# Kernel optimization log

Hardware: AMD Instinct MI355X
Metric: run time of the kernel (lower is better)

The kernel has to match this reference:

```python
import jax, jax.numpy as jnp
import numpy as np

# Static graph-batch geometry: B graphs, N nodes each (contiguous), DEG avg degree.
B, N, DEG = 128, 512, 16
GID, GH = 128, 128      # g_in_dim, g_hidden_dim
CID, CE = 64, 64        # c_in_dim, c_embed_dim
HAZ = 256               # haz_dim
K1, K2, K3 = 256, 128, 64


def _gcn(x, src, dst, mask, W, b, n):
    # GCN layer with self loops over masked (surviving) nodes; masked-out nodes contribute nothing.
    h = x @ W  # [n, GH]
    w = mask[src] * mask[dst]                                  # edge alive iff both endpoints alive
    deg = mask + jax.ops.segment_sum(w, dst, num_segments=n)    # +mask = self loop
    dinv = jax.lax.rsqrt(jnp.maximum(deg, 1.0))
    norm = w * dinv[src] * dinv[dst]
    agg = jax.ops.segment_sum(norm[:, None] * h[src], dst, num_segments=n)
    self_term = h * (mask * dinv * dinv)[:, None]               # self-loop norm = 1/deg
    return (agg + self_term + b) * mask[:, None]


def _pool(x, mask, p, k):
    # Score-based top-k pooling (MVPool score -> gate -> keep top ratio per graph), mask-based for static shapes.
    score = jax.nn.sigmoid((x @ p) / jnp.sqrt(jnp.sum(p * p)))  # [B*N]
    s = jnp.where(mask > 0, score, -jnp.inf).reshape(B, N)
    _, idx = jax.lax.top_k(s, k)                                 # [B, k]
    new_mask = jnp.zeros((B, N), x.dtype).at[jnp.arange(B)[:, None], idx].set(1.0).reshape(-1)
    x = x * (score * new_mask)[:, None]
    return x, new_mask


def _readout(x, mask):
    # readout='both': concat(global_max_pool, global_mean_pool) per graph.
    xm = x.reshape(B, N, -1)
    m = mask.reshape(B, N, 1)
    mx = jnp.max(jnp.where(m > 0, xm, -1e30), axis=1)
    avg = jnp.sum(xm * m, axis=1) / jnp.maximum(jnp.sum(m, axis=1), 1.0)
    return jnp.concatenate([mx, avg], axis=1)


def _forward(x, inp_c, src, dst, W1, b1, W2, b2, W3, b3, p1, p2, p3, We, Wa, ba, Wb, bb, Wc):
    n = B * N
    mask = jnp.ones((n,), x.dtype)
    x = jax.nn.relu(_gcn(x, src, dst, mask, W1, b1, n))
    x, mask = _pool(x, mask, p1, K1)
    x1 = _readout(x, mask)
    x = jax.nn.relu(_gcn(x, src, dst, mask, W2, b2, n))
    x, mask = _pool(x, mask, p2, K2)
    x2 = _readout(x, mask)
    x = jax.nn.relu(_gcn(x, src, dst, mask, W3, b3, n))
    x, mask = _pool(x, mask, p3, K3)
    x3 = _readout(x, mask)
    hg = jax.nn.relu(x1) + jax.nn.relu(x2) + jax.nn.relu(x3)     # [B, 2*GH]
    embed = jax.nn.relu(inp_c @ We)                               # [B, CE]
    fusion = jnp.concatenate([embed, hg], axis=1)                 # [B, 320]
    h = jax.nn.relu(fusion @ Wa + ba)                             # dropout skipped (eval mode)
    h = jax.nn.relu(h @ Wb + bb)
    return h @ Wc                                                 # out_dim=1 -> Identity


def setup_inputs() -> dict:
    key = jax.random.key(0)
    ks = jax.random.split(key, 16)
    n = B * N
    x = jax.random.normal(ks[0], (n, GID), jnp.float32)
    inp_c = jax.random.normal(ks[1], (B, CID), jnp.float32)
    offs = (jnp.arange(B, dtype=jnp.int32) * N)[:, None]
    src = (jax.random.randint(ks[2], (B, N * DEG), 0, N, jnp.int32) + offs).reshape(-1)
    dst = (jax.random.randint(ks[3], (B, N * DEG), 0, N, jnp.int32) + offs).reshape(-1)
    edge_index = jnp.stack([src, dst])
    batch = jnp.arange(n, dtype=jnp.int32) // N
    def lin(k, i, o):
        return jax.random.normal(k, (i, o), jnp.float32) / np.float32(np.sqrt(i))
    return dict(
        x=x, inp_c=inp_c, edge_index=edge_index, batch=batch,
        W1=lin(ks[4], GID, GH), b1=jnp.zeros((GH,), jnp.float32),
        W2=lin(ks[5], GH, GH), b2=jnp.zeros((GH,), jnp.float32),
        W3=lin(ks[6], GH, GH), b3=jnp.zeros((GH,), jnp.float32),
        p1=jax.random.normal(ks[7], (GH,), jnp.float32),
        p2=jax.random.normal(ks[8], (GH,), jnp.float32),
        p3=jax.random.normal(ks[9], (GH,), jnp.float32),
        We=lin(ks[10], CID, CE),
        Wa=lin(ks[11], 2 * GH + CE, HAZ), ba=jnp.zeros((HAZ,), jnp.float32),
        Wb=lin(ks[12], HAZ, HAZ // 2), bb=jnp.zeros((HAZ // 2,), jnp.float32),
        Wc=lin(ks[13], HAZ // 2, 1),
    )


def reference(x, inp_c, edge_index, batch, W1, b1, W2, b2, W3, b3, p1, p2, p3, We, Wa, ba, Wb, bb, Wc):
    # batch is implicitly arange(n)//N (contiguous equal-size graphs); reductions use the reshape form.
    src, dst = edge_index[0], edge_index[1]
    return _forward(x, inp_c, src, dst, W1, b1, W2, b2, W3, b3, p1, p2, p3, We, Wa, ba, Wb, bb, Wc)
```

## Files before the change

kernel.cpp:

```cpp
#include <hip/hip_runtime.h>
#include <math.h>

#define NNODE 65536
#define NEDGE 1048576
#define NGRAPH 128
#define NPG 512
#define EPG 8192

typedef _Float16 f16x8 __attribute__((ext_vector_type(8)));
typedef _Float16 f16x4 __attribute__((ext_vector_type(4)));
typedef float f32x4 __attribute__((ext_vector_type(4)));


__global__ __launch_bounds__(512) void k_csr(const int* __restrict__ srcE, const int* __restrict__ dstE,
                                             int* __restrict__ rp, int* __restrict__ csr,
                                             float* __restrict__ gate, int* __restrict__ alive,
                                             float* __restrict__ dinv, float* __restrict__ hg,
                                             const float* __restrict__ W0, const float* __restrict__ W1,
                                             const float* __restrict__ W2, _Float16* __restrict__ wh,
                                             _Float16* __restrict__ wl,
                                             const float* __restrict__ p0, const float* __restrict__ p1,
                                             const float* __restrict__ p2, float* __restrict__ qinv) {
    __shared__ int cnt[512];
    __shared__ int wsum[8];
    int t = threadIdx.x;
    if (blockIdx.x >= 128) {
        int vb = (blockIdx.x - 128) * 2 + (t >> 8);
        int tt = t & 255;
        if (vb == 192) {
            if (tt < 192) {
                int w = tt >> 6, lane = tt & 63;
                const float* P = (w == 0) ? p0 : (w == 1) ? p1 : p2;
                float s = P[lane] * P[lane] + P[lane + 64] * P[lane + 64];
                for (int m = 32; m >= 1; m >>= 1) s += __shfl_xor(s, m);
                if (lane == 0) qinv[w] = rsqrtf(s);
            }
        } else if (vb < 192) {
            int l = vb >> 6;
            int e = (vb & 63) * 256 + tt;
            const float* W = (l == 0) ? W0 : (l == 1) ? W1 : W2;
            int k = e >> 7, n = e & 127;
            float w = W[e];
            _Float16 hi = (_Float16)w;
            _Float16 lo = (_Float16)((w - (float)hi) * 2048.0f);
            int nt = n >> 4, nn = n & 15, ks = k >> 5, quad = (k & 31) >> 3, j = k & 7;
            int off = l * 16384 + ((nt * 4 + ks) * 64 + (quad * 16 + nn)) * 8 + j;
            wh[off] = hi;
            wl[off] = lo;
        }
        return;
    }
    int g = blockIdx.x;
    int nd = g * NPG + t;
    cnt[t] = 0;
    gate[nd] = 1.f;
    alive[nd] = nd;
    if (t < 256) hg[g * 256 + t] = 0.f;
    __syncthreads();
    int ebase = g * EPG;
    int dl[16];
    for (int i = 0; i < 16; ++i) {
        int e = ebase + t + i * 512;
        int d = dstE[e] - g * NPG;
        dl[i] = d;
        atomicAdd(&cnt[d], 1);
    }
    __syncthreads();
    int v = cnt[t];
    dinv[nd] = rsqrtf(1.f + (float)v);
    int lane = t & 63, wid = t >> 6;
    int x = v;
    for (int o = 1; o < 64; o <<= 1) {
        int n = __shfl_up(x, o);
        if (lane >= o) x += n;
    }
    if (lane == 63) wsum[wid] = x;
    __syncthreads();
    if (t == 0) {
        int run = 0;
        for (int i = 0; i < 8; ++i) { int s = wsum[i]; wsum[i] = run; run += s; }
    }
    __syncthreads();
    int incl = x + wsum[wid];
    int excl = incl - v;
    rp[nd] = ebase + excl;
    if (g == NGRAPH - 1 && t == 511) rp[NNODE] = NEDGE;
    cnt[t] = excl;
    __syncthreads();
    for (int i = 0; i < 16; ++i) {
        int e = ebase + t + i * 512;
        int pos = atomicAdd(&cnt[dl[i]], 1);
        csr[ebase + pos] = srcE[e];
    }
}


#define CVT8(hi8, lo8, a0, a1, a2, a3, a4, a5, a6, a7)                         \
    {                                                                           \
        _Float16 q0 = (_Float16)a0, q1 = (_Float16)a1, q2 = (_Float16)a2,       \
                 q3 = (_Float16)a3, q4 = (_Float16)a4, q5 = (_Float16)a5,       \
                 q6 = (_Float16)a6, q7 = (_Float16)a7;                          \
        hi8 = (f16x8){q0, q1, q2, q3, q4, q5, q6, q7};                          \
        lo8 = (f16x8){(_Float16)((a0 - (float)q0) * 2048.f),                    \
                      (_Float16)((a1 - (float)q1) * 2048.f),                    \
                      (_Float16)((a2 - (float)q2) * 2048.f),                    \
                      (_Float16)((a3 - (float)q3) * 2048.f),                    \
                      (_Float16)((a4 - (float)q4) * 2048.f),                    \
                      (_Float16)((a5 - (float)q5) * 2048.f),                    \
                      (_Float16)((a6 - (float)q6) * 2048.f),                    \
                      (_Float16)((a7 - (float)q7) * 2048.f)};                   \
    }

__global__ __launch_bounds__(256, 2) void k_gemm(const float* __restrict__ x0, const _Float16* __restrict__ xh,
                                                 const _Float16* __restrict__ xl, const _Float16* __restrict__ wh,
                                                 const _Float16* __restrict__ wl, const float* __restrict__ gate,
                                                 const int* __restrict__ alive, float* __restrict__ h,
                                                 int srcF32, int perg) {
    __shared__ _Float16 aH[128 * 72];
    __shared__ _Float16 aL[128 * 72];
    __shared__ _Float16 bH[8192];
    __shared__ _Float16 bL[8192];
    int t = threadIdx.x;
    int lane = t & 63;
    int wv = t >> 6;
    int quad = lane >> 4, mm = lane & 15;
    int gg = blockIdx.x & 127;
    int cc0 = blockIdx.x >> 7;
    int rowbase = gg * perg + cc0 * 128;

    f32x4 accH[2][8], accM[2][8];
    for (int a = 0; a < 2; ++a)
        for (int b = 0; b < 8; ++b) {
            accH[a][b] = (f32x4){0.f, 0.f, 0.f, 0.f};
            accM[a][b] = (f32x4){0.f, 0.f, 0.f, 0.f};
        }

    for (int kh = 0; kh < 2; ++kh) {
        if (kh) __syncthreads();
        for (int pp = 0; pp < 4; ++pp) {
            int seg = t + pp * 256;
            int nt = seg >> 7, ksl = (seg >> 6) & 1, ln = seg & 63;
            int goff = ((nt * 4 + kh * 2 + ksl) * 64 + ln) * 8;
            *(uint4*)(bH + seg * 8) = *(const uint4*)(wh + goff);
            *(uint4*)(bL + seg * 8) = *(const uint4*)(wl + goff);
        }
        for (int pp = 0; pp < 4; ++pp) {
            int c = t + pp * 256;
            int r = c >> 3, ch = c & 7;
            int node = alive[rowbase + r];
            size_t src = (size_t)node * 128 + kh * 64 + ch * 8;
            f16x8 hi8, lo8;
            if (srcF32) {
                float4 v0 = *(const float4*)(x0 + src);
                float4 v1 = *(const float4*)(x0 + src + 4);
                CVT8(hi8, lo8, v0.x, v0.y, v0.z, v0.w, v1.x, v1.y, v1.z, v1.w);
            } else {
                hi8 = *(const f16x8*)(xh + src);
                lo8 = *(const f16x8*)(xl + src);
            }
            *(f16x8*)(aH + r * 72 + ch * 8) = hi8;
            *(f16x8*)(aL + r * 72 + ch * 8) = lo8;
        }
        __syncthreads();

        for (int ksl = 0; ksl < 2; ++ksl) {
            f16x8 Ah[2], Al[2];
            for (int mt = 0; mt < 2; ++mt) {
                int row = wv * 32 + mt * 16 + mm;
                Ah[mt] = *(const f16x8*)(aH + row * 72 + ksl * 32 + quad * 8);
                Al[mt] = *(const f16x8*)(aL + row * 72 + ksl * 32 + quad * 8);
            }
            for (int nt = 0; nt < 8; ++nt) {
                f16x8 Bh = *(const f16x8*)(bH + ((nt * 2 + ksl) * 64 + lane) * 8);
                f16x8 Bl = *(const f16x8*)(bL + ((nt * 2 + ksl) * 64 + lane) * 8);
                for (int mt = 0; mt < 2; ++mt) {
                    accH[mt][nt] = __builtin_amdgcn_mfma_f32_16x16x32_f16(Ah[mt], Bh, accH[mt][nt], 0, 0, 0);
                    accM[mt][nt] = __builtin_amdgcn_mfma_f32_16x16x32_f16(Ah[mt], Bl, accM[mt][nt], 0, 0, 0);
                    accM[mt][nt] = __builtin_amdgcn_mfma_f32_16x16x32_f16(Al[mt], Bh, accM[mt][nt], 0, 0, 0);
                }
            }
        }
    }

    for (int mt = 0; mt < 2; ++mt)
        for (int i = 0; i < 4; ++i) {
            int rl = wv * 32 + mt * 16 + quad * 4 + i;
            int node = alive[rowbase + rl];
            float g = gate[node];
            float* hr = h + (size_t)node * 128 + mm;
            for (int nt = 0; nt < 8; ++nt)
                hr[nt * 16] = g * (accH[mt][nt][i] + accM[mt][nt][i] * (1.f / 2048.f));
        }
}


__global__ __launch_bounds__(1024) void k_aggL(const float* __restrict__ h, const float* __restrict__ dinv,
                                               const int* __restrict__ rp, const int* __restrict__ csr,
                                               const int* __restrict__ alive, const float* __restrict__ bias,
                                               const float* __restrict__ p, _Float16* __restrict__ xh,
                                               _Float16* __restrict__ xl, float* __restrict__ spart, int Kp) {
    __shared__ float hsl[512 * 68];
    __shared__ float dinv_l[512];
    __shared__ float2 nbw[64][16];
    __shared__ float bias_l[64];
    __shared__ float p_l[64];
    int t = threadIdx.x;
    int g = blockIdx.x & 127;
    int fh = blockIdx.x >> 7;
    int fb = fh * 64;
    int gbase = g * NPG;

    for (int r0 = 0; r0 < 512; r0 += 128) {
        int r = r0 + (t >> 3);
        int f8 = (t & 7) * 8;
        const float* src = h + (size_t)(gbase + r) * 128 + fb + f8;
        float4 v0 = *(const float4*)(src);
        float4 v1 = *(const float4*)(src + 4);
        *(float4*)(hsl + r * 68 + f8) = v0;
        *(float4*)(hsl + r * 68 + f8 + 4) = v1;
    }
    if (t < 512) dinv_l[t] = dinv[gbase + t];
    if (t < 64) { bias_l[t] = bias[fb + t]; p_l[t] = p[fb + t]; }
    __syncthreads();

    int lane16 = t & 15;
    int qid = t >> 4;

    for (int idx = qid; idx < Kp; idx += 64) {
        int d = alive[g * Kp + idx];
        int rd = d - gbase;
        int jb = rp[d], je = rp[d + 1];
        float dvd = dinv_l[rd];
        float4 hd = *(const float4*)(hsl + rd * 68 + lane16 * 4);
        float4 acc;
        acc.x = dvd * hd.x; acc.y = dvd * hd.y; acc.z = dvd * hd.z; acc.w = dvd * hd.w;

        for (int bk = jb; bk < je; bk += 16) {
            int nk = je - bk; if (nk > 16) nk = 16;
            float wv = 0.f;
            int rs = rd;
            if (lane16 < nk) {
                rs = csr[bk + lane16] - gbase;
                wv = dinv_l[rs];
            }
            nbw[qid][lane16] = make_float2(wv, __int_as_float(rs));
            int nk4 = (nk + 3) & ~3;
            for (int k = 0; k < nk4; k += 4) {
                float2 e0 = nbw[qid][k];
                float2 e1 = nbw[qid][k + 1];
                float2 e2 = nbw[qid][k + 2];
                float2 e3 = nbw[qid][k + 3];
                float4 h0 = *(const float4*)(hsl + __float_as_int(e0.y) * 68 + lane16 * 4);
                float4 h1 = *(const float4*)(hsl + __float_as_int(e1.y) * 68 + lane16 * 4);
                float4 h2 = *(const float4*)(hsl + __float_as_int(e2.y) * 68 + lane16 * 4);
                float4 h3 = *(const float4*)(hsl + __float_as_int(e3.y) * 68 + lane16 * 4);
                acc.x = fmaf(e0.x, h0.x, acc.x); acc.y = fmaf(e0.x, h0.y, acc.y);
                acc.z = fmaf(e0.x, h0.z, acc.z); acc.w = fmaf(e0.x, h0.w, acc.w);
                acc.x = fmaf(e1.x, h1.x, acc.x); acc.y = fmaf(e1.x, h1.y, acc.y);
                acc.z = fmaf(e1.x, h1.z, acc.z); acc.w = fmaf(e1.x, h1.w, acc.w);
                acc.x = fmaf(e2.x, h2.x, acc.x); acc.y = fmaf(e2.x, h2.y, acc.y);
                acc.z = fmaf(e2.x, h2.z, acc.z); acc.w = fmaf(e2.x, h2.w, acc.w);
                acc.x = fmaf(e3.x, h3.x, acc.x); acc.y = fmaf(e3.x, h3.y, acc.y);
                acc.z = fmaf(e3.x, h3.z, acc.z); acc.w = fmaf(e3.x, h3.w, acc.w);
            }
        }

        float4 b4 = *(const float4*)(bias_l + lane16 * 4);
        float4 o;
        o.x = fmaxf(fmaf(dvd, acc.x, b4.x), 0.f);
        o.y = fmaxf(fmaf(dvd, acc.y, b4.y), 0.f);
        o.z = fmaxf(fmaf(dvd, acc.z, b4.z), 0.f);
        o.w = fmaxf(fmaf(dvd, acc.w, b4.w), 0.f);

        _Float16 q0 = (_Float16)o.x, q1 = (_Float16)o.y, q2 = (_Float16)o.z, q3 = (_Float16)o.w;
        f16x4 oh = {q0, q1, q2, q3};
        f16x4 ol = {(_Float16)((o.x - (float)q0) * 2048.f), (_Float16)((o.y - (float)q1) * 2048.f),
                    (_Float16)((o.z - (float)q2) * 2048.f), (_Float16)((o.w - (float)q3) * 2048.f)};
        *(f16x4*)(xh + (size_t)d * 128 + fb + lane16 * 4) = oh;
        *(f16x4*)(xl + (size_t)d * 128 + fb + lane16 * 4) = ol;

        float4 p4 = *(const float4*)(p_l + lane16 * 4);
        float ps = o.x * p4.x + o.y * p4.y + o.z * p4.z + o.w * p4.w;
        ps += __shfl_xor(ps, 1);
        ps += __shfl_xor(ps, 2);
        ps += __shfl_xor(ps, 4);
        ps += __shfl_xor(ps, 8);
        if (lane16 == 0) spart[(size_t)fh * NNODE + d] = ps;
    }
}


__global__ __launch_bounds__(1024) void k_aggS(const float* __restrict__ h, const float* __restrict__ dinv,
                                               const int* __restrict__ rp, const int* __restrict__ csr,
                                               const int* __restrict__ alive, const float* __restrict__ bias,
                                               const float* __restrict__ p, _Float16* __restrict__ xh,
                                               _Float16* __restrict__ xl, float* __restrict__ spart, int Kp) {
    __shared__ float slab[256 * 68];
    __shared__ float dinv_l[512];
    __shared__ int   map_l[512];
    __shared__ float2 nbw[64][16];
    __shared__ float bias_l[64];
    __shared__ float p_l[64];
    int t = threadIdx.x;
    int g = blockIdx.x & 127;
    int fh = blockIdx.x >> 7;
    int fb = fh * 64;
    int gbase = g * NPG;

    if (t < 512) { dinv_l[t] = dinv[gbase + t]; map_l[t] = 0; }
    if (t < 64) { bias_l[t] = bias[fb + t]; p_l[t] = p[fb + t]; }
    for (int r0 = 0; r0 < Kp; r0 += 128) {
        int r = r0 + (t >> 3);
        if (r < Kp) {
            int node = alive[g * Kp + r];
            int f8 = (t & 7) * 8;
            const float* src = h + (size_t)node * 128 + fb + f8;
            float4 v0 = *(const float4*)(src);
            float4 v1 = *(const float4*)(src + 4);
            *(float4*)(slab + r * 68 + f8) = v0;
            *(float4*)(slab + r * 68 + f8 + 4) = v1;
        }
    }
    __syncthreads();
    if (t < Kp) map_l[alive[g * Kp + t] - gbase] = t;
    __syncthreads();

    int lane16 = t & 15;
    int qid = t >> 4;

    for (int idx = qid; idx < Kp; idx += 64) {
        int d = alive[g * Kp + idx];
        int rd = d - gbase;
        int jb = rp[d], je = rp[d + 1];
        float dvd = dinv_l[rd];
        float4 hd = *(const float4*)(slab + idx * 68 + lane16 * 4);
        float4 acc;
        acc.x = dvd * hd.x; acc.y = dvd * hd.y; acc.z = dvd * hd.z; acc.w = dvd * hd.w;

        for (int bk = jb; bk < je; bk += 16) {
            int nk = je - bk; if (nk > 16) nk = 16;
            float wv = 0.f;
            int sl = idx;
            if (lane16 < nk) {
                int rs = csr[bk + lane16] - gbase;
                wv = dinv_l[rs];
                sl = map_l[rs];
            }
            nbw[qid][lane16] = make_float2(wv, __int_as_float(sl));
            int nk4 = (nk + 3) & ~3;
            for (int k = 0; k < nk4; k += 4) {
                float2 e0 = nbw[qid][k];
                float2 e1 = nbw[qid][k + 1];
                float2 e2 = nbw[qid][k + 2];
                float2 e3 = nbw[qid][k + 3];
                float4 h0 = *(const float4*)(slab + __float_as_int(e0.y) * 68 + lane16 * 4);
                float4 h1 = *(const float4*)(slab + __float_as_int(e1.y) * 68 + lane16 * 4);
                float4 h2 = *(const float4*)(slab + __float_as_int(e2.y) * 68 + lane16 * 4);
                float4 h3 = *(const float4*)(slab + __float_as_int(e3.y) * 68 + lane16 * 4);
                acc.x = fmaf(e0.x, h0.x, acc.x); acc.y = fmaf(e0.x, h0.y, acc.y);
                acc.z = fmaf(e0.x, h0.z, acc.z); acc.w = fmaf(e0.x, h0.w, acc.w);
                acc.x = fmaf(e1.x, h1.x, acc.x); acc.y = fmaf(e1.x, h1.y, acc.y);
                acc.z = fmaf(e1.x, h1.z, acc.z); acc.w = fmaf(e1.x, h1.w, acc.w);
                acc.x = fmaf(e2.x, h2.x, acc.x); acc.y = fmaf(e2.x, h2.y, acc.y);
                acc.z = fmaf(e2.x, h2.z, acc.z); acc.w = fmaf(e2.x, h2.w, acc.w);
                acc.x = fmaf(e3.x, h3.x, acc.x); acc.y = fmaf(e3.x, h3.y, acc.y);
                acc.z = fmaf(e3.x, h3.z, acc.z); acc.w = fmaf(e3.x, h3.w, acc.w);
            }
        }

        float4 b4 = *(const float4*)(bias_l + lane16 * 4);
        float4 o;
        o.x = fmaxf(fmaf(dvd, acc.x, b4.x), 0.f);
        o.y = fmaxf(fmaf(dvd, acc.y, b4.y), 0.f);
        o.z = fmaxf(fmaf(dvd, acc.z, b4.z), 0.f);
        o.w = fmaxf(fmaf(dvd, acc.w, b4.w), 0.f);

        _Float16 q0 = (_Float16)o.x, q1 = (_Float16)o.y, q2 = (_Float16)o.z, q3 = (_Float16)o.w;
        f16x4 oh = {q0, q1, q2, q3};
        f16x4 ol = {(_Float16)((o.x - (float)q0) * 2048.f), (_Float16)((o.y - (float)q1) * 2048.f),
                    (_Float16)((o.z - (float)q2) * 2048.f), (_Float16)((o.w - (float)q3) * 2048.f)};
        *(f16x4*)(xh + (size_t)d * 128 + fb + lane16 * 4) = oh;
        *(f16x4*)(xl + (size_t)d * 128 + fb + lane16 * 4) = ol;

        float4 p4 = *(const float4*)(p_l + lane16 * 4);
        float ps = o.x * p4.x + o.y * p4.y + o.z * p4.z + o.w * p4.w;
        ps += __shfl_xor(ps, 1);
        ps += __shfl_xor(ps, 2);
        ps += __shfl_xor(ps, 4);
        ps += __shfl_xor(ps, 8);
        if (lane16 == 0) spart[(size_t)fh * NNODE + d] = ps;
    }
}


__device__ __forceinline__ void pool_body(const _Float16* __restrict__ xh, const _Float16* __restrict__ xl,
                                          const float* __restrict__ spart, const float* __restrict__ qinv,
                                          int lidx, float* __restrict__ gate,
                                          int* __restrict__ alive, float* __restrict__ hg,
                                          const int* __restrict__ rp, const int* __restrict__ csr,
                                          float* __restrict__ dinv, int K, int last, int g, int t) {
    __shared__ unsigned hist[1024];
    __shared__ unsigned wsum[8];
    __shared__ float cand[512];
    __shared__ int ad[256];
    __shared__ float ag[256];
    __shared__ float red[1024];
    __shared__ int m_new[512];
    __shared__ int scnt;
    __shared__ unsigned ccnt;
    __shared__ unsigned tbb, tbab;
    __shared__ float thrS;
    int gbase = g * NPG;
    int d = gbase + t;

    float odv = dinv[d];
    int m = odv > 0.f;
    float z = spart[d] + spart[NNODE + d];
    float sc = 1.f / (1.f + expf(-z * qinv[lidx]));
    unsigned bits = m ? __float_as_uint(sc) : 0u;
    unsigned bucket = bits >> 21;
    hist[t] = 0; hist[t + 512] = 0;
    if (t == 0) { scnt = 0; ccnt = 0; }
    __syncthreads();
    atomicAdd(&hist[bucket], 1u);
    __syncthreads();
    unsigned a0 = hist[1023 - 2 * t];
    unsigned a1 = hist[1022 - 2 * t];
    unsigned pair = a0 + a1;
    unsigned v = pair;
    for (int o = 1; o < 64; o <<= 1) {
        unsigned n = __shfl_up(v, o);
        if ((t & 63) >= o) v += n;
    }
    if ((t & 63) == 63) wsum[t >> 6] = v;
    __syncthreads();
    if (t == 0) {
        unsigned run = 0;
        for (int i = 0; i < 8; ++i) { unsigned x = wsum[i]; wsum[i] = run; run += x; }
    }
    __syncthreads();
    unsigned incl = v + wsum[t >> 6];
    unsigned excl = incl - pair;
    unsigned uK = (unsigned)K;
    if (excl < uK && excl + a0 >= uK) { tbb = 1023 - 2 * t; tbab = excl; }
    else if (excl + a0 < uK && incl >= uK) { tbb = 1022 - 2 * t; tbab = excl + a0; }
    __syncthreads();
    unsigned bsel = tbb;
    unsigned r = uK - tbab;
    if (m && bucket == bsel) {
        unsigned pos = atomicAdd(&ccnt, 1u);
        cand[pos] = sc;
    }
    __syncthreads();
    unsigned c = ccnt;
    if (t < (int)c) {
        float vv = cand[t];
        unsigned gt = 0;
        for (unsigned i = 0; i < c; ++i) gt += (cand[i] > vv) ? 1u : 0u;
        if (gt == r - 1) thrS = vv;
    }
    __syncthreads();
    float thr = thrS;

    int nm = (m && sc >= thr) ? 1 : 0;
    gate[d] = nm ? sc : 0.f;
    m_new[t] = nm;
    if (nm) {
        int pos = atomicAdd(&scnt, 1);
        if (pos < K) {
            alive[g * K + pos] = d;
            ad[pos] = d;
            ag[pos] = sc;
        }
    }
    __syncthreads();

    if (!last) {
        float nd = 0.f;
        if (nm) {
            int jb = rp[d], je = rp[d + 1];
            int sum = 0;
            for (int j = jb; j < je; ++j) sum += m_new[csr[j] - gbase];
            nd = rsqrtf(1.f + (float)sum);
        }
        dinv[d] = nd;
    }

    int f = t & 127, c2 = t >> 7;
    float mx = 0.f, sm = 0.f;
#define REC(node) ((float)xh[(size_t)(node)*128 + f] + (float)xl[(size_t)(node)*128 + f] * (1.f / 2048.f))
    for (int j = c2; j < K; j += 16) {
        float v0 = REC(ad[j]) * ag[j];
        float v1 = REC(ad[j + 4]) * ag[j + 4];
        float v2 = REC(ad[j + 8]) * ag[j + 8];
        float v3 = REC(ad[j + 12]) * ag[j + 12];
        mx = fmaxf(fmaxf(fmaxf(mx, v0), fmaxf(v1, v2)), v3);
        sm += v0 + v1 + v2 + v3;
    }
#undef REC
    red[t] = mx; red[512 + t] = sm;
    __syncthreads();
    if (c2 == 0) {
        for (int cc = 1; cc < 4; ++cc) {
            mx = fmaxf(mx, red[cc * 128 + f]);
            sm += red[512 + cc * 128 + f];
        }
        hg[g * 256 + f] += mx;
        hg[g * 256 + 128 + f] += sm / (float)K;
    }
}


__global__ __launch_bounds__(512) void k_poolA(const _Float16* __restrict__ xh, const _Float16* __restrict__ xl,
                                               const float* __restrict__ spart, const float* __restrict__ qinv,
                                               int lidx, float* __restrict__ gate,
                                               int* __restrict__ alive, float* __restrict__ hg,
                                               const int* __restrict__ rp, const int* __restrict__ csr,
                                               float* __restrict__ dinv, int K, int last) {
    pool_body(xh, xl, spart, qinv, lidx, gate, alive, hg, rp, csr, dinv, K, last,
              blockIdx.x, threadIdx.x);
}


__global__ __launch_bounds__(512) void k_poolB(const _Float16* __restrict__ xh, const _Float16* __restrict__ xl,
                                               const float* __restrict__ spart, const float* __restrict__ qinv,
                                               int lidx, float* __restrict__ gate,
                                               int* __restrict__ alive, float* __restrict__ hg,
                                               const int* __restrict__ rp, const int* __restrict__ csr,
                                               float* __restrict__ dinv, int K, int last,
                                               const _Float16* __restrict__ wh3, const _Float16* __restrict__ wl3,
                                               float* __restrict__ h) {
    __shared__ _Float16 aH[128 * 72];
    __shared__ _Float16 aL[128 * 72];
    __shared__ _Float16 bH[8192];
    __shared__ _Float16 bL[8192];
    int t = threadIdx.x, g = blockIdx.x;
    pool_body(xh, xl, spart, qinv, lidx, gate, alive, hg, rp, csr, dinv, K, last, g, t);
    __syncthreads();

    int lane = t & 63;
    int wv = t >> 6;
    int quad = lane >> 4, mm = lane & 15;
    int rowbase = g * 128;

    f32x4 accH[2][8], accM[2][8];
    for (int a = 0; a < 2; ++a)
        for (int b = 0; b < 8; ++b) {
            accH[a][b] = (f32x4){0.f, 0.f, 0.f, 0.f};
            accM[a][b] = (f32x4){0.f, 0.f, 0.f, 0.f};
        }

    for (int kh = 0; kh < 2; ++kh) {
        if (kh) __syncthreads();
        for (int pp = 0; pp < 2; ++pp) {
            int seg = t + pp * 512;
            int nt = seg >> 7, ksl = (seg >> 6) & 1, ln = seg & 63;
            int goff = ((nt * 4 + kh * 2 + ksl) * 64 + ln) * 8;
            *(uint4*)(bH + seg * 8) = *(const uint4*)(wh3 + goff);
            *(uint4*)(bL + seg * 8) = *(const uint4*)(wl3 + goff);
        }
        for (int pp = 0; pp < 2; ++pp) {
            int c = t + pp * 512;
            int r = c >> 3, ch = c & 7;
            int node = alive[rowbase + r];
            size_t src = (size_t)node * 128 + kh * 64 + ch * 8;
            *(f16x8*)(aH + r * 72 + ch * 8) = *(const f16x8*)(xh + src);
            *(f16x8*)(aL + r * 72 + ch * 8) = *(const f16x8*)(xl + src);
        }
        __syncthreads();

        if (t < 256) {
            for (int ksl = 0; ksl < 2; ++ksl) {
                f16x8 Ah[2], Al[2];
                for (int mt = 0; mt < 2; ++mt) {
                    int row = wv * 32 + mt * 16 + mm;
                    Ah[mt] = *(const f16x8*)(aH + row * 72 + ksl * 32 + quad * 8);
                    Al[mt] = *(const f16x8*)(aL + row * 72 + ksl * 32 + quad * 8);
                }
                for (int nt = 0; nt < 8; ++nt) {
                    f16x8 Bh = *(const f16x8*)(bH + ((nt * 2 + ksl) * 64 + lane) * 8);
                    f16x8 Bl = *(const f16x8*)(bL + ((nt * 2 + ksl) * 64 + lane) * 8);
                    for (int mt = 0; mt < 2; ++mt) {
                        accH[mt][nt] = __builtin_amdgcn_mfma_f32_16x16x32_f16(Ah[mt], Bh, accH[mt][nt], 0, 0, 0);
                        accM[mt][nt] = __builtin_amdgcn_mfma_f32_16x16x32_f16(Ah[mt], Bl, accM[mt][nt], 0, 0, 0);
                        accM[mt][nt] = __builtin_amdgcn_mfma_f32_16x16x32_f16(Al[mt], Bh, accM[mt][nt], 0, 0, 0);
                    }
                }
            }
        }
    }

    if (t < 256) {
        for (int mt = 0; mt < 2; ++mt)
            for (int i = 0; i < 4; ++i) {
                int rl = wv * 32 + mt * 16 + quad * 4 + i;
                int node = alive[rowbase + rl];
                float gg = gate[node];
                float* hr = h + (size_t)node * 128 + mm;
                for (int nt = 0; nt < 8; ++nt)
                    hr[nt * 16] = gg * (accH[mt][nt][i] + accM[mt][nt][i] * (1.f / 2048.f));
            }
    }
}


__global__ __launch_bounds__(512) void k_poolC(const _Float16* __restrict__ xh, const _Float16* __restrict__ xl,
                                               const float* __restrict__ spart, const float* __restrict__ qinv,
                                               int lidx, float* __restrict__ gate,
                                               int* __restrict__ alive, float* __restrict__ hg,
                                               const int* __restrict__ rp, const int* __restrict__ csr,
                                               float* __restrict__ dinv, int K, int last,
                                               const float* __restrict__ inp_c,
                                               const float* __restrict__ We, const float* __restrict__ Wa,
                                               const float* __restrict__ ba, const float* __restrict__ Wb,
                                               const float* __restrict__ bb, const float* __restrict__ Wc,
                                               float* __restrict__ out) {
    __shared__ float fus[320];
    __shared__ float h1[256];
    __shared__ float h2[128];
    int t = threadIdx.x, g = blockIdx.x;
    pool_body(xh, xl, spart, qinv, lidx, gate, alive, hg, rp, csr, dinv, K, last, g, t);
    __syncthreads();

    if (t < 64) {
        float a = 0.f;
        for (int j = 0; j < 64; ++j) a = fmaf(inp_c[g * 64 + j], We[j * 64 + t], a);
        fus[t] = fmaxf(a, 0.f);
    }
    if (t < 256) fus[64 + t] = hg[g * 256 + t];
    __syncthreads();
    if (t < 256) {
        float a = ba[t];
        for (int j = 0; j < 320; ++j) a = fmaf(fus[j], Wa[j * 256 + t], a);
        h1[t] = fmaxf(a, 0.f);
    }
    __syncthreads();
    if (t < 128) {
        float a = bb[t];
        for (int j = 0; j < 256; ++j) a = fmaf(h1[j], Wb[j * 128 + t], a);
        h2[t] = fmaxf(a, 0.f);
    }
    __syncthreads();
    if (t == 0) {
        float a = 0.f;
        for (int j = 0; j < 128; ++j) a = fmaf(h2[j], Wc[j], a);
        out[g] = a;
    }
}


extern "C" void kernel_launch(void* const* d_in, const int* in_sizes, int n_in,
                              void* d_out, int out_size, void* d_ws, size_t ws_size,
                              hipStream_t stream) {
    (void)in_sizes; (void)n_in; (void)out_size; (void)ws_size;
    const float* x_in  = (const float*)d_in[0];
    const float* inp_c = (const float*)d_in[1];
    const int*   ei    = (const int*)d_in[2];
    const int* srcE = ei;
    const int* dstE = ei + NEDGE;
    const float* Wl[3] = {(const float*)d_in[4], (const float*)d_in[6], (const float*)d_in[8]};
    const float* bl[3] = {(const float*)d_in[5], (const float*)d_in[7], (const float*)d_in[9]};
    const float* Pl[3] = {(const float*)d_in[10], (const float*)d_in[11], (const float*)d_in[12]};
    const float* We = (const float*)d_in[13];
    const float* Wa = (const float*)d_in[14];
    const float* ba = (const float*)d_in[15];
    const float* Wb = (const float*)d_in[16];
    const float* bb = (const float*)d_in[17];
    const float* Wc = (const float*)d_in[18];
    float* out = (float*)d_out;

    char* w = (char*)d_ws;
    size_t off = 0;
    auto alloc = [&](size_t bytes) -> void* {
        void* p = w + off;
        off = (off + bytes + 255) & ~(size_t)255;
        return p;
    };
    int*   rp    = (int*)alloc((NNODE + 1) * 4);
    int*   csr   = (int*)alloc(NEDGE * 4);
    float* dinv  = (float*)alloc(NNODE * 4);
    float* gate  = (float*)alloc(NNODE * 4);
    float* spart = (float*)alloc((size_t)2 * NNODE * 4);
    float* qinv  = (float*)alloc(256);
    int*   alive = (int*)alloc(NNODE * 4);
    float* hbuf  = (float*)alloc((size_t)NNODE * 128 * 4);
    _Float16* xh = (_Float16*)alloc((size_t)NNODE * 128 * 2);
    _Float16* xl = (_Float16*)alloc((size_t)NNODE * 128 * 2);
    float* hg    = (float*)alloc(NGRAPH * 256 * 4);
    _Float16* wfh = (_Float16*)alloc(3 * 16384 * 2);
    _Float16* wfl = (_Float16*)alloc(3 * 16384 * 2);

    k_csr<<<225, 512, 0, stream>>>(srcE, dstE, rp, csr, gate, alive, dinv, hg,
                                   Wl[0], Wl[1], Wl[2], wfh, wfl, Pl[0], Pl[1], Pl[2], qinv);

    k_gemm<<<512, 256, 0, stream>>>(x_in, xh, xl, wfh, wfl, gate, alive, hbuf, 1, 512);
    k_aggL<<<256, 1024, 0, stream>>>(hbuf, dinv, rp, csr, alive, bl[0], Pl[0], xh, xl, spart, 512);
    k_poolA<<<NGRAPH, 512, 0, stream>>>(xh, xl, spart, qinv, 0, gate, alive, hg, rp, csr, dinv, 256, 0);

    k_gemm<<<256, 256, 0, stream>>>(x_in, xh, xl, wfh + 16384, wfl + 16384, gate, alive, hbuf, 0, 256);
    k_aggS<<<256, 1024, 0, stream>>>(hbuf, dinv, rp, csr, alive, bl[1], Pl[1], xh, xl, spart, 256);
    k_poolB<<<NGRAPH, 512, 0, stream>>>(xh, xl, spart, qinv, 1, gate, alive, hg, rp, csr, dinv, 128, 0,
                                        wfh + 32768, wfl + 32768, hbuf);

    k_aggS<<<256, 1024, 0, stream>>>(hbuf, dinv, rp, csr, alive, bl[2], Pl[2], xh, xl, spart, 128);
    k_poolC<<<NGRAPH, 512, 0, stream>>>(xh, xl, spart, qinv, 2, gate, alive, hg, rp, csr, dinv, 64, 1,
                                        inp_c, We, Wa, ba, Wb, bb, Wc, out);
}
```

Before: 263.0 us.

## Fuse layer-2 feature GEMM into first pooling kernel

The first pooling kernel now also computes the layer-2 GEMM for its graph's 256 surviving nodes. It gathers their split-f16 features and the weight fragments into shared memory, runs MFMA with hi/lo error compensation, and writes the gated result to hbuf. This removes a separate k_gemm launch and the global round-trip between pooling and the GEMM. The cost is that only 128 blocks with large LDS footprints (~106KB) do the GEMM, instead of 256 blocks, which may reduce parallelism.

```diff
diff --git a/kernel.cpp b/kernel.cpp
--- a/kernel.cpp
+++ b/kernel.cpp
@@ -516,9 +516,76 @@
                                                int lidx, float* __restrict__ gate,
                                                int* __restrict__ alive, float* __restrict__ hg,
                                                const int* __restrict__ rp, const int* __restrict__ csr,
-                                               float* __restrict__ dinv, int K, int last) {
-    pool_body(xh, xl, spart, qinv, lidx, gate, alive, hg, rp, csr, dinv, K, last,
-              blockIdx.x, threadIdx.x);
+                                               float* __restrict__ dinv, int K, int last,
+                                               const _Float16* __restrict__ wh2, const _Float16* __restrict__ wl2,
+                                               float* __restrict__ h) {
+    __shared__ _Float16 aH[256 * 72];
+    __shared__ _Float16 aL[256 * 72];
+    __shared__ _Float16 bH[8192];
+    __shared__ _Float16 bL[8192];
+    int t = threadIdx.x, g = blockIdx.x;
+    pool_body(xh, xl, spart, qinv, lidx, gate, alive, hg, rp, csr, dinv, K, last, g, t);
+    __syncthreads();
+
+    int lane = t & 63;
+    int wv = t >> 6;
+    int quad = lane >> 4, mm = lane & 15;
+    int rowbase = g * 256;
+
+    f32x4 accH[2][8], accM[2][8];
+    for (int a = 0; a < 2; ++a)
+        for (int b = 0; b < 8; ++b) {
+            accH[a][b] = (f32x4){0.f, 0.f, 0.f, 0.f};
+            accM[a][b] = (f32x4){0.f, 0.f, 0.f, 0.f};
+        }
+
+    for (int kh = 0; kh < 2; ++kh) {
+        if (kh) __syncthreads();
+        for (int pp = 0; pp < 2; ++pp) {
+            int seg = t + pp * 512;
+            int nt = seg >> 7, ksl = (seg >> 6) & 1, ln = seg & 63;
+            int goff = ((nt * 4 + kh * 2 + ksl) * 64 + ln) * 8;
+            *(uint4*)(bH + seg * 8) = *(const uint4*)(wh2 + goff);
+            *(uint4*)(bL + seg * 8) = *(const uint4*)(wl2 + goff);
+        }
+        for (int pp = 0; pp < 4; ++pp) {
+            int c = t + pp * 512;
+            int r = c >> 3, ch = c & 7;
+            int node = alive[rowbase + r];
+            size_t src = (size_t)node * 128 + kh * 64 + ch * 8;
+            *(f16x8*)(aH + r * 72 + ch * 8) = *(const f16x8*)(xh + src);
+            *(f16x8*)(aL + r * 72 + ch * 8) = *(const f16x8*)(xl + src);
+        }
+        __syncthreads();
+
+        for (int ksl = 0; ksl < 2; ++ksl) {
+            f16x8 Ah[2], Al[2];
+            for (int mt = 0; mt < 2; ++mt) {
+                int row = wv * 32 + mt * 16 + mm;
+                Ah[mt] = *(const f16x8*)(aH + row * 72 + ksl * 32 + quad * 8);
+                Al[mt] = *(const f16x8*)(aL + row * 72 + ksl * 32 + quad * 8);
+            }
+            for (int nt = 0; nt < 8; ++nt) {
+                f16x8 Bh = *(const f16x8*)(bH + ((nt * 2 + ksl) * 64 + lane) * 8);
+                f16x8 Bl = *(const f16x8*)(bL + ((nt * 2 + ksl) * 64 + lane) * 8);
+                for (int mt = 0; mt < 2; ++mt) {
+                    accH[mt][nt] = __builtin_amdgcn_mfma_f32_16x16x32_f16(Ah[mt], Bh, accH[mt][nt], 0, 0, 0);
+                    accM[mt][nt] = __builtin_amdgcn_mfma_f32_16x16x32_f16(Ah[mt], Bl, accM[mt][nt], 0, 0, 0);
+                    accM[mt][nt] = __builtin_amdgcn_mfma_f32_16x16x32_f16(Al[mt], Bh, accM[mt][nt], 0, 0, 0);
+                }
+            }
+        }
+    }
+
+    for (int mt = 0; mt < 2; ++mt)
+        for (int i = 0; i < 4; ++i) {
+            int rl = wv * 32 + mt * 16 + quad * 4 + i;
+            int node = alive[rowbase + rl];
+            float gg = gate[node];
+            float* hr = h + (size_t)node * 128 + mm;
+            for (int nt = 0; nt < 8; ++nt)
+                hr[nt * 16] = gg * (accH[mt][nt][i] + accM[mt][nt][i] * (1.f / 2048.f));
+        }
 }
 
 
@@ -695,9 +762,9 @@
 
     k_gemm<<<512, 256, 0, stream>>>(x_in, xh, xl, wfh, wfl, gate, alive, hbuf, 1, 512);
     k_aggL<<<256, 1024, 0, stream>>>(hbuf, dinv, rp, csr, alive, bl[0], Pl[0], xh, xl, spart, 512);
-    k_poolA<<<NGRAPH, 512, 0, stream>>>(xh, xl, spart, qinv, 0, gate, alive, hg, rp, csr, dinv, 256, 0);
-
-    k_gemm<<<256, 256, 0, stream>>>(x_in, xh, xl, wfh + 16384, wfl + 16384, gate, alive, hbuf, 0, 256);
+    k_poolA<<<NGRAPH, 512, 0, stream>>>(xh, xl, spart, qinv, 0, gate, alive, hg, rp, csr, dinv, 256, 0,
+                                        wfh + 16384, wfl + 16384, hbuf);
+
     k_aggS<<<256, 1024, 0, stream>>>(hbuf, dinv, rp, csr, alive, bl[1], Pl[1], xh, xl, spart, 256);
     k_poolB<<<NGRAPH, 512, 0, stream>>>(xh, xl, spart, qinv, 1, gate, alive, hg, rp, csr, dinv, 128, 0,
                                         wfh + 32768, wfl + 32768, hbuf);
```

Measured after the change: 268.4 us. 2.0% more time.
